# Optimization experiments

Measured on AMD Instinct MI355X. Metric: run time of the kernel, lower is better.

Reference implementation:

```python
import jax, jax.numpy as jnp
import numpy as np

B, N, D = 16, 2048, 1024


def _linear_params(key, d, scale):
    kw, kb = jax.random.split(key)
    W = jax.random.uniform(kw, (d, d), jnp.float32, -scale, scale)
    b = jax.random.uniform(kb, (d,), jnp.float32, -scale, scale)
    return W, b


def setup_inputs() -> dict:
    key = jax.random.key(0)
    ks = jax.random.split(key, 9)
    scale = 1.0 / np.sqrt(D)  # torch nn.Linear default init range
    x1 = jax.random.normal(ks[0], (B, N, D), jnp.float32)
    x2 = jax.random.normal(ks[1], (B, N, D), jnp.float32)
    Wq, bq = _linear_params(ks[2], D, scale)
    Wk, bk = _linear_params(ks[3], D, scale)
    Wv, bv = _linear_params(ks[4], D, scale)
    W1, b1 = _linear_params(ks[5], D, scale)
    W2, b2 = _linear_params(ks[6], D, scale)
    W3, b3 = _linear_params(ks[7], D, scale)
    # torch init is zeros(1); use small nonzero so output/grad paths are exercised
    gamma = jax.random.normal(ks[8], (1,), jnp.float32) * 0.1
    return {"x1": x1, "x2": x2, "Wq": Wq, "bq": bq, "Wk": Wk, "bk": bk,
            "Wv": Wv, "bv": bv, "W1": W1, "b1": b1, "W2": W2, "b2": b2,
            "W3": W3, "b3": b3, "gamma": gamma}


def reference(x1, x2, Wq, bq, Wk, bk, Wv, bv, W1, b1, W2, b2, W3, b3, gamma):
    # QKV cross-attention (unscaled softmax, as in the torch source)
    q = jnp.einsum('bnd,ed->bne', x1, Wq) + bq
    k = jnp.einsum('bnd,ed->bne', x2, Wk) + bk
    v = jnp.einsum('bnd,ed->bne', x2, Wv) + bv
    energy = jnp.einsum('bik,bjk->bij', q, k)          # [B, N, N]
    attn = jax.nn.softmax(energy, axis=-1)
    out = jnp.einsum('bij,bjk->bik', attn, v)          # [B, N, D]
    # multiscale sigmoid gate: sigmoid(s1 + s2 + s3)
    s = (jnp.einsum('bnd,ed->bne', out, W1) + b1
         + jnp.einsum('bnd,ed->bne', out, W2) + b2
         + jnp.einsum('bnd,ed->bne', out, W3) + b3)
    out = out * jax.nn.sigmoid(s)
    return gamma * out + x1
```

## Files before the change

kernel.cpp:

```cpp
#include <hip/hip_runtime.h>
#include <hip/hip_bf16.h>
#include <hip/hip_fp16.h>
#include <cstdint>

#define B_ 16
#define N_ 2048
#define D_ 1024

typedef __attribute__((ext_vector_type(4))) float f32x4;
typedef __attribute__((ext_vector_type(8))) short s16x8;

typedef __attribute__((address_space(1))) const void* gas_ptr;
typedef __attribute__((address_space(3))) void* las_ptr;

__device__ __forceinline__ void gload16(const void* g, void* l)
{
    __builtin_amdgcn_global_load_lds((gas_ptr)(uintptr_t)g, (las_ptr)(uintptr_t)l, 16, 0, 0);
}

__device__ __forceinline__ ushort f2bf(float f)
{
    union { __hip_bfloat16 h; ushort u; } c;
    c.h = __float2bfloat16(f);
    return c.u;
}
__device__ __forceinline__ float bf2f(ushort u)
{
    union { __hip_bfloat16 h; ushort u; } c;
    c.u = u;
    return __bfloat162float(c.h);
}

__global__ __launch_bounds__(256)
void cvt_bf16(const float* __restrict__ in, ushort* __restrict__ out, long n)
{
    long i = ((long)blockIdx.x * 256 + threadIdx.x) * 8;
    const long stride = (long)gridDim.x * 256 * 8;
    for (; i < n; i += stride) {
        f32x4 a = *(const f32x4*)(in + i);
        f32x4 b = *(const f32x4*)(in + i + 4);
        s16x8 o;
#pragma unroll
        for (int j = 0; j < 4; ++j) { o[j] = (short)f2bf(a[j]); o[4 + j] = (short)f2bf(b[j]); }
        *(s16x8*)(out + i) = o;
    }
}

__global__ __launch_bounds__(256)
void prep_w(const float* __restrict__ Wq, const float* __restrict__ Wk, const float* __restrict__ Wv,
            const float* __restrict__ W1, const float* __restrict__ W2, const float* __restrict__ W3,
            const float* __restrict__ b1, const float* __restrict__ b2, const float* __restrict__ b3,
            ushort* __restrict__ wq, ushort* __restrict__ wk, ushort* __restrict__ wv,
            ushort* __restrict__ wsum, float* __restrict__ bsum)
{
    const long i = ((long)blockIdx.x * 256 + threadIdx.x) * 4;
    if (i < (long)D_ * D_) {
#pragma unroll
        for (int j = 0; j < 4; ++j) {
            wq[i + j] = f2bf(Wq[i + j]);
            wk[i + j] = f2bf(Wk[i + j]);
            wv[i + j] = f2bf(Wv[i + j]);
            wsum[i + j] = f2bf(W1[i + j] + W2[i + j] + W3[i + j]);
        }
        if (i < D_) {
#pragma unroll
            for (int j = 0; j < 4; ++j) bsum[i + j] = b1[i + j] + b2[i + j] + b3[i + j];
        }
    }
}

template<int EPI>
__global__ __launch_bounds__(512, 2)
void gemm256(const ushort* __restrict__ A, const ushort* __restrict__ Bw,
             void* __restrict__ Out, const float* __restrict__ bias,
             int Nn, int K, int NT,
             long sA, long sB, long sO,
             const ushort* __restrict__ outb, const float* __restrict__ x1r,
             const float* __restrict__ gamma)
{
    __shared__ ushort lds[65536];
    const int tid = threadIdx.x;
    const int l = tid & 63;
    const int w = tid >> 6;
    const int wm = w >> 2, wn = w & 3;
    const int lr = l & 15;
    const int c2x = ((((l >> 4) * 16) ^ ((lr & 8) << 2)) >> 1);

    const int gx = gridDim.x, gy = gridDim.y;
    const int nwg = gx * gy * (int)gridDim.z;
    const int orig = ((int)blockIdx.z * gy + blockIdx.y) * gx + blockIdx.x;
    const int swzb = (orig & 7) * (nwg >> 3) + (orig >> 3);
    const int gxy = gx * gy;
    const int bz = swzb / gxy;
    const int rem = swzb - bz * gxy;
    const int by = rem / gx;
    const int bx = rem - by * gx;
    const int m0 = by * 256, n0 = bx * 256;

    const ushort* Ab = A + (long)bz * sA;
    const ushort* Bb = Bw + (long)bz * sB;

    int srow[2], scol[2];
#pragma unroll
    for (int i = 0; i < 2; ++i) {
        const int L = (i * 512 + tid) * 16;
        const int P = L ^ (((L >> 9) & 1) << 5);
        srow[i] = (P >> 6) & 127;
        scol[i] = ((P >> 13) << 5) | ((P & 63) >> 1);
    }
    const int sdst = w * 512;

    f32x4 acc[8][4];
#pragma unroll
    for (int i = 0; i < 8; ++i)
#pragma unroll
        for (int j = 0; j < 4; ++j) acc[i][j] = f32x4{0.f, 0.f, 0.f, 0.f};
    s16x8 a[4][2], b[2][2][2];

#define STAGEH(pl, t)                                                                     \
    if ((t) < NT) {                                                                       \
        const int rb2 = (t) & 1;                                                          \
        const long kk = (long)(t) << 6;                                                   \
        _Pragma("unroll")                                                                 \
        for (int i = 0; i < 2; ++i) {                                                     \
            if ((pl) < 2)                                                                 \
                gload16(Ab + (long)(m0 + (pl) * 128 + srow[i]) * K + kk + scol[i],        \
                        &lds[rb2 * 16384 + (pl) * 8192 + sdst + i * 4096]);               \
            else                                                                          \
                gload16(Bb + (long)(n0 + ((pl) - 2) * 128 + srow[i]) * K + kk + scol[i],  \
                        &lds[32768 + rb2 * 16384 + ((pl) - 2) * 8192 + sdst + i * 4096]); \
        }                                                                                 \
    }

#define LDA_(qm)                                                                           \
    _Pragma("unroll") for (int mi = 0; mi < 4; ++mi)                                       \
    _Pragma("unroll") for (int ks = 0; ks < 2; ++ks)                                       \
        a[mi][ks] = *(const s16x8*)&lds[rbase_a + ks * 4096 + ((qm) * 64 + mi * 16 + lr) * 32 + c2x];

#define LDB_(qn)                                                                           \
    _Pragma("unroll") for (int ni = 0; ni < 2; ++ni)                                       \
    _Pragma("unroll") for (int ks = 0; ks < 2; ++ks)                                       \
        b[qn][ni][ks] = *(const s16x8*)&lds[rbase_b + ks * 4096 +                          \
            ((wn & 1) * 64 + (qn) * 32 + ni * 16 + lr) * 32 + c2x];

#define MM_(qm, qn)                                                                        \
    __builtin_amdgcn_s_setprio(1);                                                         \
    _Pragma("unroll") for (int mi = 0; mi < 4; ++mi)                                       \
    _Pragma("unroll") for (int ni = 0; ni < 2; ++ni)                                       \
    _Pragma("unroll") for (int ks = 0; ks < 2; ++ks)                                       \
        acc[(qm) * 4 + mi][(qn) * 2 + ni] = __builtin_amdgcn_mfma_f32_16x16x32_bf16(       \
            a[mi][ks], b[qn][ni][ks], acc[(qm) * 4 + mi][(qn) * 2 + ni], 0, 0, 0);         \
    __builtin_amdgcn_s_setprio(0);

#define BARR __builtin_amdgcn_s_barrier()
#define LGKM0 do { asm volatile("s_waitcnt lgkmcnt(0)" ::: "memory"); \
                   __builtin_amdgcn_sched_barrier(0); } while (0)

#define KGROUP(tt, VMSTR) {                                          \
    const int rb = (tt) & 1;                                         \
    const int rbase_a = rb * 16384 + wm * 8192;                      \
    const int rbase_b = 32768 + rb * 16384 + (wn >> 1) * 8192;       \
                                                            \
    LDB_(0); LDA_(0);                                                \
    STAGEH(1, (tt) + 1);                                             \
    BARR; LGKM0; MM_(0, 0); BARR;                                    \
                                                            \
    LDB_(1);                                                         \
    STAGEH(2, (tt) + 1);                                             \
    BARR; LGKM0; MM_(0, 1); BARR;                                    \
                                                            \
    LDA_(1);                                                         \
    STAGEH(3, (tt) + 1);                                             \
    BARR; LGKM0; MM_(1, 0); BARR;                                    \
     \
    MM_(1, 1);                                                       \
    STAGEH(0, (tt) + 2);                                             \
    asm volatile("s_waitcnt " VMSTR ::: "memory");                   \
    BARR; }

    STAGEH(0, 0); STAGEH(1, 0); STAGEH(2, 0); STAGEH(3, 0);
    STAGEH(0, 1);
    asm volatile("s_waitcnt vmcnt(2)" ::: "memory");
    BARR;

    int t = 0;
    for (; t < NT - 2; ++t) KGROUP(t, "vmcnt(2)");
    for (; t < NT; ++t) KGROUP(t, "vmcnt(0)");

#undef KGROUP
#undef STAGEH
#undef LDA_
#undef LDB_
#undef MM_

    float gam = 0.f;
    if (EPI == 3) gam = *gamma;
#pragma unroll
    for (int am = 0; am < 8; ++am) {
#pragma unroll
        for (int an = 0; an < 4; ++an) {
#pragma unroll
            for (int r = 0; r < 4; ++r) {
                const int m = m0 + wm * 128 + am * 16 + (l >> 4) * 4 + r;
                const int n = n0 + wn * 64 + an * 16 + lr;
                const float v = acc[am][an][r];
                const long o = (long)bz * sO + (long)m * Nn + n;
                if (EPI == 0) {
                    ((ushort*)Out)[o] = f2bf(v + bias[n]);
                } else if (EPI == 1) {
                    union { __half h; ushort u; } c;
                    c.h = __float2half(v);
                    ((ushort*)Out)[o] = c.u;
                } else if (EPI == 2) {
                    ((ushort*)Out)[o] = f2bf(v);
                } else {
                    const float s = v + bias[n];
                    const float g = 1.f / (1.f + __expf(-s));
                    const float ov = bf2f(outb[(long)m * Nn + n]);
                    ((float*)Out)[o] = gam * ov * g + x1r[(long)m * Nn + n];
                }
            }
        }
    }
}

__global__ __launch_bounds__(256)
void transpose_v(const ushort* __restrict__ V, ushort* __restrict__ Vt)
{
    const int z = blockIdx.z;
    const int j0 = blockIdx.x * 64;
    const int d0 = blockIdx.y * 64;
    __shared__ ushort tile[64][72];
    const int t = threadIdx.x;
    const int r = t >> 2;
    const int cq = (t & 3) * 16;
    const ushort* vb = V + (long)z * N_ * D_;
    ushort* vtb = Vt + (long)z * D_ * N_;
#pragma unroll
    for (int i = 0; i < 2; ++i) {
        s16x8 x = *(const s16x8*)(vb + (long)(j0 + r) * D_ + d0 + cq + i * 8);
        *(s16x8*)&tile[r][cq + i * 8] = x;
    }
    __syncthreads();
#pragma unroll
    for (int i = 0; i < 2; ++i) {
        s16x8 ov;
#pragma unroll
        for (int jj = 0; jj < 8; ++jj) ov[jj] = (short)tile[cq + i * 8 + jj][r];
        *(s16x8*)(vtb + (long)(d0 + r) * N_ + j0 + cq + i * 8) = ov;
    }
}

__global__ __launch_bounds__(256)
void softmax_inplace(ushort* __restrict__ EA)
{
    const long row = blockIdx.x;
    ushort* p = EA + row * N_;
    const int tid = threadIdx.x;
    const int c0 = tid * 8;
    __shared__ float red[8];

    s16x8 raw = *(const s16x8*)(p + c0);
    float v[8];
    float mx = -3.0e38f;
#pragma unroll
    for (int i = 0; i < 8; ++i) {
        union { ushort u; __half h; } c;
        c.u = (ushort)raw[i];
        v[i] = __half2float(c.h);
        mx = fmaxf(mx, v[i]);
    }
#pragma unroll
    for (int off = 32; off > 0; off >>= 1) mx = fmaxf(mx, __shfl_xor(mx, off));
    if ((tid & 63) == 0) red[tid >> 6] = mx;
    __syncthreads();
    mx = fmaxf(fmaxf(red[0], red[1]), fmaxf(red[2], red[3]));

    float s = 0.f;
#pragma unroll
    for (int i = 0; i < 8; ++i) { v[i] = __expf(v[i] - mx); s += v[i]; }
#pragma unroll
    for (int off = 32; off > 0; off >>= 1) s += __shfl_xor(s, off);
    if ((tid & 63) == 0) red[4 + (tid >> 6)] = s;
    __syncthreads();
    s = (red[4] + red[5]) + (red[6] + red[7]);
    const float inv = 1.f / s;

    s16x8 o;
#pragma unroll
    for (int i = 0; i < 8; ++i) o[i] = (short)f2bf(v[i] * inv);
    *(s16x8*)(p + c0) = o;
}

extern "C" void kernel_launch(void* const* d_in, const int* in_sizes, int n_in,
                              void* d_out, int out_size, void* d_ws, size_t ws_size,
                              hipStream_t stream)
{
    const float* x1 = (const float*)d_in[0];
    const float* x2 = (const float*)d_in[1];
    const float* Wq = (const float*)d_in[2];
    const float* bq = (const float*)d_in[3];
    const float* Wk = (const float*)d_in[4];
    const float* bk = (const float*)d_in[5];
    const float* Wv = (const float*)d_in[6];
    const float* bv = (const float*)d_in[7];
    const float* W1 = (const float*)d_in[8];
    const float* b1 = (const float*)d_in[9];
    const float* W2 = (const float*)d_in[10];
    const float* b2 = (const float*)d_in[11];
    const float* W3 = (const float*)d_in[12];
    const float* b3 = (const float*)d_in[13];
    const float* gamma = (const float*)d_in[14];
    float* out = (float*)d_out;

    char* ws = (char*)d_ws;
    const long SZ_XB = (long)B_ * N_ * D_ * 2;
    ushort* x1b  = (ushort*)(ws);
    ushort* x2b  = (ushort*)(ws + SZ_XB);
    ushort* EA   = (ushort*)(ws);
    ushort* wqb  = (ushort*)(ws + 2 * SZ_XB);
    ushort* wkb  = (ushort*)(ws + 2 * SZ_XB + 1L * 2097152);
    ushort* wvb  = (ushort*)(ws + 2 * SZ_XB + 2L * 2097152);
    ushort* wsb  = (ushort*)(ws + 2 * SZ_XB + 3L * 2097152);
    float*  bsum = (float*) (ws + 2 * SZ_XB + 4L * 2097152);
    char* base2  = ws + 2 * SZ_XB + 4L * 2097152 + 4096;
    ushort* Qb   = (ushort*)(base2);
    ushort* Kb   = (ushort*)(base2 + SZ_XB);
    ushort* Vb   = (ushort*)(base2 + 2 * SZ_XB);
    ushort* Vtb  = Qb;
    ushort* outb = Kb;

    const long NE = (long)B_ * N_ * D_;

    cvt_bf16<<<4096, 256, 0, stream>>>(x1, x1b, NE);
    cvt_bf16<<<4096, 256, 0, stream>>>(x2, x2b, NE);
    prep_w<<<1024, 256, 0, stream>>>(Wq, Wk, Wv, W1, W2, W3, b1, b2, b3,
                                     wqb, wkb, wvb, wsb, bsum);

    gemm256<0><<<dim3(4, 128, 1), 512, 0, stream>>>(x1b, wqb, Qb, bq,
        D_, D_, 16, 0, 0, 0, nullptr, nullptr, nullptr);
    gemm256<0><<<dim3(4, 128, 1), 512, 0, stream>>>(x2b, wkb, Kb, bk,
        D_, D_, 16, 0, 0, 0, nullptr, nullptr, nullptr);
    gemm256<0><<<dim3(4, 128, 1), 512, 0, stream>>>(x2b, wvb, Vb, bv,
        D_, D_, 16, 0, 0, 0, nullptr, nullptr, nullptr);

    gemm256<1><<<dim3(8, 8, 16), 512, 0, stream>>>(Qb, Kb, EA, nullptr,
        N_, D_, 16, (long)N_ * D_, (long)N_ * D_, (long)N_ * N_,
        nullptr, nullptr, nullptr);

    transpose_v<<<dim3(32, 16, 16), 256, 0, stream>>>(Vb, Vtb);

    softmax_inplace<<<B_ * N_, 256, 0, stream>>>(EA);

    gemm256<2><<<dim3(4, 8, 16), 512, 0, stream>>>(EA, Vtb, outb, nullptr,
        D_, N_, 32, (long)N_ * N_, (long)D_ * N_, (long)N_ * D_,
        nullptr, nullptr, nullptr);

    gemm256<3><<<dim3(4, 128, 1), 512, 0, stream>>>(outb, wsb, out, bsum,
        D_, D_, 16, 0, 0, 0, outb, x1, gamma);
}
```

Before: 762.9 us.

## Compute V transposed directly via swapped GEMM and deepen load prefetch

After: 739.0 us. 3.1% less time.

```diff
diff --git a/kernel.cpp b/kernel.cpp
--- a/kernel.cpp
+++ b/kernel.cpp
@@ -162,29 +162,29 @@
     const int rbase_b = 32768 + rb * 16384 + (wn >> 1) * 8192;       \
                                                             \
     LDB_(0); LDA_(0);                                                \
-    STAGEH(1, (tt) + 1);                                             \
     BARR; LGKM0; MM_(0, 0); BARR;                                    \
-                                                            \
+                                 \
     LDB_(1);                                                         \
-    STAGEH(2, (tt) + 1);                                             \
     BARR; LGKM0; MM_(0, 1); BARR;                                    \
-                                                            \
+               \
     LDA_(1);                                                         \
-    STAGEH(3, (tt) + 1);                                             \
+    STAGEH(2, (tt) + 2);                                             \
+    STAGEH(3, (tt) + 2);                                             \
     BARR; LGKM0; MM_(1, 0); BARR;                                    \
-     \
+               \
     MM_(1, 1);                                                       \
     STAGEH(0, (tt) + 2);                                             \
+    STAGEH(1, (tt) + 2);                                             \
     asm volatile("s_waitcnt " VMSTR ::: "memory");                   \
     BARR; }
 
     STAGEH(0, 0); STAGEH(1, 0); STAGEH(2, 0); STAGEH(3, 0);
-    STAGEH(0, 1);
-    asm volatile("s_waitcnt vmcnt(2)" ::: "memory");
+    STAGEH(0, 1); STAGEH(1, 1); STAGEH(2, 1); STAGEH(3, 1);
+    asm volatile("s_waitcnt vmcnt(8)" ::: "memory");
     BARR;
 
     int t = 0;
-    for (; t < NT - 2; ++t) KGROUP(t, "vmcnt(2)");
+    for (; t < NT - 2; ++t) KGROUP(t, "vmcnt(8)");
     for (; t < NT; ++t) KGROUP(t, "vmcnt(0)");
 
 #undef KGROUP
@@ -213,6 +213,8 @@
                     ((ushort*)Out)[o] = c.u;
                 } else if (EPI == 2) {
                     ((ushort*)Out)[o] = f2bf(v);
+                } else if (EPI == 4) {
+                    ((ushort*)Out)[o] = f2bf(v + bias[m]);
                 } else {
                     const float s = v + bias[n];
                     const float g = 1.f / (1.f + __expf(-s));
@@ -221,33 +223,6 @@
                 }
             }
         }
-    }
-}
-
-__global__ __launch_bounds__(256)
-void transpose_v(const ushort* __restrict__ V, ushort* __restrict__ Vt)
-{
-    const int z = blockIdx.z;
-    const int j0 = blockIdx.x * 64;
-    const int d0 = blockIdx.y * 64;
-    __shared__ ushort tile[64][72];
-    const int t = threadIdx.x;
-    const int r = t >> 2;
-    const int cq = (t & 3) * 16;
-    const ushort* vb = V + (long)z * N_ * D_;
-    ushort* vtb = Vt + (long)z * D_ * N_;
-#pragma unroll
-    for (int i = 0; i < 2; ++i) {
-        s16x8 x = *(const s16x8*)(vb + (long)(j0 + r) * D_ + d0 + cq + i * 8);
-        *(s16x8*)&tile[r][cq + i * 8] = x;
-    }
-    __syncthreads();
-#pragma unroll
-    for (int i = 0; i < 2; ++i) {
-        s16x8 ov;
-#pragma unroll
-        for (int jj = 0; jj < 8; ++jj) ov[jj] = (short)tile[cq + i * 8 + jj][r];
-        *(s16x8*)(vtb + (long)(d0 + r) * N_ + j0 + cq + i * 8) = ov;
     }
 }
 
@@ -326,8 +301,7 @@
     char* base2  = ws + 2 * SZ_XB + 4L * 2097152 + 4096;
     ushort* Qb   = (ushort*)(base2);
     ushort* Kb   = (ushort*)(base2 + SZ_XB);
-    ushort* Vb   = (ushort*)(base2 + 2 * SZ_XB);
-    ushort* Vtb  = Qb;
+    ushort* Vtb  = (ushort*)(base2 + 2 * SZ_XB);
     ushort* outb = Kb;
 
     const long NE = (long)B_ * N_ * D_;
@@ -341,15 +315,15 @@
         D_, D_, 16, 0, 0, 0, nullptr, nullptr, nullptr);
     gemm256<0><<<dim3(4, 128, 1), 512, 0, stream>>>(x2b, wkb, Kb, bk,
         D_, D_, 16, 0, 0, 0, nullptr, nullptr, nullptr);
-    gemm256<0><<<dim3(4, 128, 1), 512, 0, stream>>>(x2b, wvb, Vb, bv,
-        D_, D_, 16, 0, 0, 0, nullptr, nullptr, nullptr);
+
+    gemm256<4><<<dim3(8, 4, 16), 512, 0, stream>>>(wvb, x2b, Vtb, bv,
+        N_, D_, 16, 0, (long)N_ * D_, (long)D_ * N_,
+        nullptr, nullptr, nullptr);
 
     gemm256<1><<<dim3(8, 8, 16), 512, 0, stream>>>(Qb, Kb, EA, nullptr,
         N_, D_, 16, (long)N_ * D_, (long)N_ * D_, (long)N_ * N_,
         nullptr, nullptr, nullptr);
 
-    transpose_v<<<dim3(32, 16, 16), 256, 0, stream>>>(Vb, Vtb);
-
     softmax_inplace<<<B_ * N_, 256, 0, stream>>>(EA);
 
     gemm256<2><<<dim3(4, 8, 16), 512, 0, stream>>>(EA, Vtb, outb, nullptr,
```
